# Kernel tuning notes

Hardware: AMD Instinct MI355X
Metric: run time of the kernel (lower is better)

## Reference

```python
import jax, jax.numpy as jnp
import numpy as np

B, D, P = 1024, 1024, 16  # batch, latent_dim(=out_dim), part_dim

def setup_inputs() -> dict:
    key = jax.random.key(0)
    k1, k2 = jax.random.split(key)
    x = jax.random.normal(k1, (B, D, P), dtype=jnp.float32)
    # per-part Linear weights, torch Linear weight shape [out, in] stacked over parts
    W = jax.random.normal(k2, (P, D, D), dtype=jnp.float32) * 0.02
    return {"x": x, "W": W}

def reference(x, W):
    # x: [B, D, P]; W: [P, O, D] (O == D here). stack_dim=-1: slice last dim,
    # apply part-specific Linear (no bias) + exact GELU, stack on last dim.
    y = jnp.einsum('bdp,pod->bop', x, W)  # grouped per-part GEMM -> [B, O, P]
    return jax.nn.gelu(y, approximate=False)
```

## Files before the change

kernel.cpp:

```cpp
#include <hip/hip_runtime.h>
#include <hip/hip_bf16.h>
#include <math.h>

typedef __hip_bfloat16 bf16;
typedef __attribute__((ext_vector_type(8))) short bf16x8;
typedef __attribute__((ext_vector_type(4))) float f32x4;
typedef __attribute__((ext_vector_type(16))) float f32x16;

#define DI static __device__ __forceinline__

constexpr int NB = 1024;
constexpr int ND = 1024;
constexpr int NP = 16;
constexpr int BKT = 32;
constexpr int NKT = ND / BKT;

DI float gelu_exact(float x) {
    return 0.5f * x * (1.0f + erff(x * 0.70710678118654752f));
}

DI ushort bf16_bits(float f) {
    bf16 h = __float2bfloat16(f);
    return *reinterpret_cast<ushort*>(&h);
}

__global__ __launch_bounds__(256) void pack_kernel(const float* __restrict__ x,
                                                   const float* __restrict__ w,
                                                   bf16* __restrict__ xp,
                                                   bf16* __restrict__ wp) {
    __shared__ ushort lds[16][264];
    const int t = threadIdx.x;
    if (blockIdx.x < 4096) {
        const int b = blockIdx.x >> 2;
        const int q = blockIdx.x & 3;
        const float* xb = x + ((size_t)b * ND + q * 256) * NP;
        float4 va[2], vb[2];
#pragma unroll
        for (int it = 0; it < 2; ++it) {
            const int u  = it * 256 + t;
            const int dh = u >> 2;
            const int p0 = (u & 3) * 4;
            va[it] = *reinterpret_cast<const float4*>(&xb[(size_t)(dh * 2)     * NP + p0]);
            vb[it] = *reinterpret_cast<const float4*>(&xb[(size_t)(dh * 2 + 1) * NP + p0]);
        }
#pragma unroll
        for (int it = 0; it < 2; ++it) {
            const int u  = it * 256 + t;
            const int dh = u >> 2;
            const int p0 = (u & 3) * 4;
            const float a0[4] = { va[it].x, va[it].y, va[it].z, va[it].w };
            const float a1[4] = { vb[it].x, vb[it].y, vb[it].z, vb[it].w };
#pragma unroll
            for (int k = 0; k < 4; ++k) {
                const uint packed = (uint)bf16_bits(a0[k]) | ((uint)bf16_bits(a1[k]) << 16);
                *reinterpret_cast<uint*>(&lds[p0 + k][dh * 2]) = packed;
            }
        }
        __syncthreads();
        const int p = t >> 4, j = t & 15;
        bf16* dst = xp + (size_t)p * (NB * ND) + (size_t)b * ND + q * 256;
#pragma unroll
        for (int it = 0; it < 2; ++it) {
            const int c = it * 16 + j;
            *reinterpret_cast<bf16x8*>(&dst[c * 8]) =
                *reinterpret_cast<const bf16x8*>(&lds[p][c * 8]);
        }
    } else {
        const size_t i = ((size_t)(blockIdx.x - 4096) * 256 + t) * 16;
        float4 f[4];
#pragma unroll
        for (int k = 0; k < 4; ++k)
            f[k] = *reinterpret_cast<const float4*>(&w[i + k * 4]);
#pragma unroll
        for (int h = 0; h < 2; ++h) {
            alignas(16) bf16 tmp[8] = {
                __float2bfloat16(f[h * 2].x),     __float2bfloat16(f[h * 2].y),
                __float2bfloat16(f[h * 2].z),     __float2bfloat16(f[h * 2].w),
                __float2bfloat16(f[h * 2 + 1].x), __float2bfloat16(f[h * 2 + 1].y),
                __float2bfloat16(f[h * 2 + 1].z), __float2bfloat16(f[h * 2 + 1].w) };
            *reinterpret_cast<bf16x8*>(&wp[i + h * 8]) = *reinterpret_cast<const bf16x8*>(tmp);
        }
    }
}

__global__ __launch_bounds__(512, 2) void gemm8_kernel(const bf16* __restrict__ xp,
                                                       const bf16* __restrict__ wp,
                                                       bf16* __restrict__ y) {
    __shared__ bf16 As[3][256 * BKT];
    __shared__ bf16 Bs[3][256 * BKT];
    const int i = blockIdx.x;
    const int p    = ((i & 7) << 1) | ((i >> 3) & 1);
    const int tile = i >> 4;
    const int bt = (tile >> 2) * 256;
    const int ot = (tile & 3) * 256;
    const bf16* A  = xp + (size_t)p * NB * ND;
    const bf16* Bm = wp + (size_t)p * ND * ND;
    const int t = threadIdx.x;
    const int l = t & 63, w = t >> 6;
    const int wr = w >> 2, wc = w & 3;
    const int lr32 = l & 31, g2 = l >> 5;

    f32x16 acc[4][2] = {};

    auto stage = [&](int buf, int kt, int q) {
        const int s   = ((q & 1) * 8 + w) * 64 + l;
        const int row = s >> 2;
        const int cb  = (s & 3) ^ ((row >> 1) & 3);
        const bf16* gsrc = (q < 2 ? A + (size_t)(bt + row) * ND
                                  : Bm + (size_t)(ot + row) * ND) + kt * BKT + cb * 8;
        bf16* ldst = (q < 2 ? &As[buf][((q & 1) * 8 + w) * 512]
                            : &Bs[buf][((q & 1) * 8 + w) * 512]);
        __builtin_amdgcn_global_load_lds((const __attribute__((address_space(1))) void*)gsrc,
                                         (__attribute__((address_space(3))) void*)ldst, 16, 0, 0);
    };
    auto readA = [&](int buf, int m, int s) -> bf16x8 {
        const int row  = wr * 128 + m * 32 + lr32;
        const int ch   = s * 2 + g2;
        const int slot = row * 4 + (ch ^ ((row >> 1) & 3));
        return *reinterpret_cast<const bf16x8*>(&As[buf][slot * 8]);
    };
    auto readB = [&](int buf, int n, int s) -> bf16x8 {
        const int row  = wc * 64 + n * 32 + lr32;
        const int ch   = s * 2 + g2;
        const int slot = row * 4 + (ch ^ ((row >> 1) & 3));
        return *reinterpret_cast<const bf16x8*>(&Bs[buf][slot * 8]);
    };

#pragma unroll
    for (int q = 0; q < 4; ++q) stage(0, 0, q);
#pragma unroll
    for (int q = 0; q < 4; ++q) stage(1, 1, q);
    asm volatile("s_waitcnt vmcnt(4)" ::: "memory");
    __builtin_amdgcn_s_barrier();
    __builtin_amdgcn_sched_barrier(0);

    int bufc = 0, bufs = 2;
#pragma unroll 1
    for (int kt = 0; kt < NKT; ++kt) {
        bf16x8 bfr[2], af[4];
#pragma unroll
        for (int n = 0; n < 2; ++n) bfr[n] = readB(bufc, n, 0);
#pragma unroll
        for (int m = 0; m < 4; ++m) af[m] = readA(bufc, m, 0);
        if (kt + 2 < NKT) { stage(bufs, kt + 2, 0); stage(bufs, kt + 2, 1); }
        __builtin_amdgcn_s_barrier();
        asm volatile("s_waitcnt lgkmcnt(0)" ::: "memory");
        __builtin_amdgcn_s_setprio(1);
#pragma unroll
        for (int m = 0; m < 4; ++m)
#pragma unroll
            for (int n = 0; n < 2; ++n)
                acc[m][n] = __builtin_amdgcn_mfma_f32_32x32x16_bf16(af[m], bfr[n], acc[m][n], 0, 0, 0);
        __builtin_amdgcn_s_setprio(0);
        __builtin_amdgcn_s_barrier();
#pragma unroll
        for (int n = 0; n < 2; ++n) bfr[n] = readB(bufc, n, 1);
#pragma unroll
        for (int m = 0; m < 4; ++m) af[m] = readA(bufc, m, 1);
        if (kt + 2 < NKT) { stage(bufs, kt + 2, 2); stage(bufs, kt + 2, 3); }
        __builtin_amdgcn_s_barrier();
        asm volatile("s_waitcnt lgkmcnt(0)" ::: "memory");
        __builtin_amdgcn_s_setprio(1);
#pragma unroll
        for (int m = 0; m < 4; ++m)
#pragma unroll
            for (int n = 0; n < 2; ++n)
                acc[m][n] = __builtin_amdgcn_mfma_f32_32x32x16_bf16(af[m], bfr[n], acc[m][n], 0, 0, 0);
        __builtin_amdgcn_s_setprio(0);
        if (kt < NKT - 1) {
            if (kt + 2 < NKT) asm volatile("s_waitcnt vmcnt(4)" ::: "memory");
            else              asm volatile("s_waitcnt vmcnt(0)" ::: "memory");
            __builtin_amdgcn_s_barrier();
            __builtin_amdgcn_sched_barrier(0);
        }
        bufc = (bufc == 2) ? 0 : bufc + 1;
        bufs = (bufs == 2) ? 0 : bufs + 1;
    }

    bf16* yp = y + (size_t)p * NB * ND;
#pragma unroll
    for (int m = 0; m < 4; ++m) {
#pragma unroll
        for (int n = 0; n < 2; ++n) {
#pragma unroll
            for (int reg = 0; reg < 16; ++reg) {
                const int row = bt + wr * 128 + m * 32 + (reg & 3) + 8 * (reg >> 2) + 4 * g2;
                const int col = ot + wc * 64 + n * 32 + lr32;
                yp[(size_t)row * ND + col] = __float2bfloat16(acc[m][n][reg]);
            }
        }
    }
}

__global__ __launch_bounds__(256) void unpack_kernel(const bf16* __restrict__ y,
                                                     float* __restrict__ out) {
    const size_t gidx = (size_t)blockIdx.x * 256 + threadIdx.x;
    const size_t o = gidx & 1023;
    const size_t b = gidx >> 10;
    const bf16* yb = y + b * (size_t)ND + o;
    float v[16];
#pragma unroll
    for (int p = 0; p < 16; ++p)
        v[p] = gelu_exact(__bfloat162float(yb[(size_t)p * (NB * ND)]));
    float4* dst = reinterpret_cast<float4*>(out + gidx * NP);
#pragma unroll
    for (int q = 0; q < 4; ++q)
        dst[q] = make_float4(v[q * 4], v[q * 4 + 1], v[q * 4 + 2], v[q * 4 + 3]);
}

__global__ __launch_bounds__(256, 4) void gemm_direct_kernel(const bf16* __restrict__ xp,
                                                             const bf16* __restrict__ wp,
                                                             float* __restrict__ out) {
    constexpr int BK = 32;
    __shared__ bf16 As[2][128 * BK];
    __shared__ bf16 Bs[2][128 * BK];
    const int i = blockIdx.x;
    const int p    = ((i & 7) << 1) | ((i >> 9) & 1);
    const int tile = (i >> 3) & 63;
    const int ot = (tile & 7) * 128;
    const int bt = (tile >> 3) * 128;
    const bf16* A  = xp + (size_t)p * NB * ND;
    const bf16* Bm = wp + (size_t)p * ND * ND;
    const int t = threadIdx.x;
    const int l = t & 63;
    const int w = t >> 6;
    const int wr = w >> 1, wc = w & 1;
    f32x4 acc[4][4] = {};
    auto stage = [&](int buf, int k0) {
#pragma unroll
        for (int r = 0; r < 2; ++r) {
            const int c   = r * 256 + t;
            const int row = c >> 2;
            const int cc  = c & 3;
            const bf16* ga = A  + (size_t)(bt + row) * ND + (k0 + cc * 8);
            const bf16* gb = Bm + (size_t)(ot + row) * ND + (k0 + cc * 8);
            bf16* la = &As[buf][(r * 256 + w * 64) * 8];
            bf16* lb = &Bs[buf][(r * 256 + w * 64) * 8];
            __builtin_amdgcn_global_load_lds((const __attribute__((address_space(1))) void*)ga,
                                             (__attribute__((address_space(3))) void*)la, 16, 0, 0);
            __builtin_amdgcn_global_load_lds((const __attribute__((address_space(1))) void*)gb,
                                             (__attribute__((address_space(3))) void*)lb, 16, 0, 0);
        }
    };
    int buf = 0;
    stage(0, 0);
    for (int kt = 0; kt < ND / BK; ++kt) {
        __syncthreads();
        if (kt + 1 < ND / BK) stage(buf ^ 1, (kt + 1) * BK);
        const int lr = l & 15;
        const int lk = (l >> 4) * 8;
        bf16x8 af[4], bfr[4];
#pragma unroll
        for (int m = 0; m < 4; ++m)
            af[m] = *reinterpret_cast<const bf16x8*>(&As[buf][(wr * 64 + m * 16 + lr) * BK + lk]);
#pragma unroll
        for (int n = 0; n < 4; ++n)
            bfr[n] = *reinterpret_cast<const bf16x8*>(&Bs[buf][(wc * 64 + n * 16 + lr) * BK + lk]);
#pragma unroll
        for (int m = 0; m < 4; ++m)
#pragma unroll
            for (int n = 0; n < 4; ++n)
                acc[m][n] = __builtin_amdgcn_mfma_f32_16x16x32_bf16(af[m], bfr[n], acc[m][n], 0, 0, 0);
        buf ^= 1;
    }
    const int lr4 = (l >> 4) * 4;
    const int lc  = l & 15;
    const int row0 = bt + wr * 64, col0 = ot + wc * 64;
#pragma unroll
    for (int m = 0; m < 4; ++m)
#pragma unroll
        for (int j = 0; j < 4; ++j) {
            const int r = row0 + m * 16 + lr4 + j;
#pragma unroll
            for (int n = 0; n < 4; ++n) {
                const int c = col0 + n * 16 + lc;
                out[((size_t)r * ND + c) * NP + p] = gelu_exact(acc[m][n][j]);
            }
        }
}

__global__ __launch_bounds__(256) void fallback_kernel(const float* __restrict__ x,
                                                       const float* __restrict__ w,
                                                       float* __restrict__ out) {
    __shared__ float As[64][17];
    __shared__ float Bs[64][17];
    const int p = blockIdx.z, bt = blockIdx.y * 64, ot = blockIdx.x * 64;
    const int t = threadIdx.x;
    const int tx = t & 15, ty = t >> 4;
    float acc[4][4] = {};
    for (int k0 = 0; k0 < ND; k0 += 16) {
        __syncthreads();
#pragma unroll
        for (int i = 0; i < 4; ++i) {
            const int idx = i * 256 + t;
            const int r = idx >> 4, k = idx & 15;
            As[r][k] = x[((size_t)(bt + r) * ND + k0 + k) * NP + p];
            Bs[r][k] = w[(size_t)p * ND * ND + (size_t)(ot + r) * ND + k0 + k];
        }
        __syncthreads();
#pragma unroll
        for (int k = 0; k < 16; ++k) {
            float a[4], bb[4];
#pragma unroll
            for (int i = 0; i < 4; ++i) a[i] = As[ty * 4 + i][k];
#pragma unroll
            for (int j = 0; j < 4; ++j) bb[j] = Bs[tx * 4 + j][k];
#pragma unroll
            for (int i = 0; i < 4; ++i)
#pragma unroll
                for (int j = 0; j < 4; ++j) acc[i][j] += a[i] * bb[j];
        }
    }
#pragma unroll
    for (int i = 0; i < 4; ++i)
#pragma unroll
        for (int j = 0; j < 4; ++j)
            out[((size_t)(bt + ty * 4 + i) * ND + (ot + tx * 4 + j)) * NP + p] =
                gelu_exact(acc[i][j]);
}

extern "C" void kernel_launch(void* const* d_in, const int* in_sizes, int n_in,
                              void* d_out, int out_size, void* d_ws, size_t ws_size,
                              hipStream_t stream) {
    const float* x = (const float*)d_in[0];
    const float* w = (const float*)d_in[1];
    float* out = (float*)d_out;

    const size_t nElem     = (size_t)NP * NB * ND;
    const size_t packBytes = nElem * sizeof(bf16) * 2;
    const size_t yBytes    = nElem * sizeof(bf16);

    if (ws_size >= packBytes) {
        bf16* xp = (bf16*)d_ws;
        bf16* wp = xp + nElem;
        pack_kernel<<<8192, 256, 0, stream>>>(x, w, xp, wp);
        if (ws_size >= packBytes + yBytes) {
            bf16* y = (bf16*)((char*)d_ws + packBytes);
            gemm8_kernel<<<256, 512, 0, stream>>>(xp, wp, y);
            unpack_kernel<<<(int)(NB * ND / 256), 256, 0, stream>>>(y, out);
        } else {
            gemm_direct_kernel<<<1024, 256, 0, stream>>>(xp, wp, out);
        }
    } else {
        fallback_kernel<<<dim3(16, 16, 16), 256, 0, stream>>>(x, w, out);
    }
}
```

Measured before the change: 112.7 us.

## Fuse weight fp32-to-bf16 conversion into GEMM B-tile staging

Drops the separate weight-packing pass. The GEMM now loads fp32 weights straight into registers, converts them to bf16, and writes them into the swizzled LDS tile, one stage ahead through two ping-pong register sets. This removes a full write and re-read of a 32MB bf16 copy of W. In exchange each GEMM block reads twice as many bytes for B, and the extra register pressure forces launch_bounds occupancy from 2 to 1.

```diff
diff --git a/kernel.cpp b/kernel.cpp
--- a/kernel.cpp
+++ b/kernel.cpp
@@ -25,66 +25,47 @@
 }
 
 __global__ __launch_bounds__(256) void pack_kernel(const float* __restrict__ x,
-                                                   const float* __restrict__ w,
-                                                   bf16* __restrict__ xp,
-                                                   bf16* __restrict__ wp) {
+                                                   bf16* __restrict__ xp) {
     __shared__ ushort lds[16][264];
     const int t = threadIdx.x;
-    if (blockIdx.x < 4096) {
-        const int b = blockIdx.x >> 2;
-        const int q = blockIdx.x & 3;
-        const float* xb = x + ((size_t)b * ND + q * 256) * NP;
-        float4 va[2], vb[2];
-#pragma unroll
-        for (int it = 0; it < 2; ++it) {
-            const int u  = it * 256 + t;
-            const int dh = u >> 2;
-            const int p0 = (u & 3) * 4;
-            va[it] = *reinterpret_cast<const float4*>(&xb[(size_t)(dh * 2)     * NP + p0]);
-            vb[it] = *reinterpret_cast<const float4*>(&xb[(size_t)(dh * 2 + 1) * NP + p0]);
-        }
-#pragma unroll
-        for (int it = 0; it < 2; ++it) {
-            const int u  = it * 256 + t;
-            const int dh = u >> 2;
-            const int p0 = (u & 3) * 4;
-            const float a0[4] = { va[it].x, va[it].y, va[it].z, va[it].w };
-            const float a1[4] = { vb[it].x, vb[it].y, vb[it].z, vb[it].w };
-#pragma unroll
-            for (int k = 0; k < 4; ++k) {
-                const uint packed = (uint)bf16_bits(a0[k]) | ((uint)bf16_bits(a1[k]) << 16);
-                *reinterpret_cast<uint*>(&lds[p0 + k][dh * 2]) = packed;
-            }
-        }
-        __syncthreads();
-        const int p = t >> 4, j = t & 15;
-        bf16* dst = xp + (size_t)p * (NB * ND) + (size_t)b * ND + q * 256;
-#pragma unroll
-        for (int it = 0; it < 2; ++it) {
-            const int c = it * 16 + j;
-            *reinterpret_cast<bf16x8*>(&dst[c * 8]) =
-                *reinterpret_cast<const bf16x8*>(&lds[p][c * 8]);
-        }
-    } else {
-        const size_t i = ((size_t)(blockIdx.x - 4096) * 256 + t) * 16;
-        float4 f[4];
-#pragma unroll
-        for (int k = 0; k < 4; ++k)
-            f[k] = *reinterpret_cast<const float4*>(&w[i + k * 4]);
-#pragma unroll
-        for (int h = 0; h < 2; ++h) {
-            alignas(16) bf16 tmp[8] = {
-                __float2bfloat16(f[h * 2].x),     __float2bfloat16(f[h * 2].y),
-                __float2bfloat16(f[h * 2].z),     __float2bfloat16(f[h * 2].w),
-                __float2bfloat16(f[h * 2 + 1].x), __float2bfloat16(f[h * 2 + 1].y),
-                __float2bfloat16(f[h * 2 + 1].z), __float2bfloat16(f[h * 2 + 1].w) };
-            *reinterpret_cast<bf16x8*>(&wp[i + h * 8]) = *reinterpret_cast<const bf16x8*>(tmp);
-        }
-    }
-}
-
-__global__ __launch_bounds__(512, 2) void gemm8_kernel(const bf16* __restrict__ xp,
-                                                       const bf16* __restrict__ wp,
+    const int b = blockIdx.x >> 2;
+    const int q = blockIdx.x & 3;
+    const float* xb = x + ((size_t)b * ND + q * 256) * NP;
+    float4 va[2], vb[2];
+#pragma unroll
+    for (int it = 0; it < 2; ++it) {
+        const int u  = it * 256 + t;
+        const int dh = u >> 2;
+        const int p0 = (u & 3) * 4;
+        va[it] = *reinterpret_cast<const float4*>(&xb[(size_t)(dh * 2)     * NP + p0]);
+        vb[it] = *reinterpret_cast<const float4*>(&xb[(size_t)(dh * 2 + 1) * NP + p0]);
+    }
+#pragma unroll
+    for (int it = 0; it < 2; ++it) {
+        const int u  = it * 256 + t;
+        const int dh = u >> 2;
+        const int p0 = (u & 3) * 4;
+        const float a0[4] = { va[it].x, va[it].y, va[it].z, va[it].w };
+        const float a1[4] = { vb[it].x, vb[it].y, vb[it].z, vb[it].w };
+#pragma unroll
+        for (int k = 0; k < 4; ++k) {
+            const uint packed = (uint)bf16_bits(a0[k]) | ((uint)bf16_bits(a1[k]) << 16);
+            *reinterpret_cast<uint*>(&lds[p0 + k][dh * 2]) = packed;
+        }
+    }
+    __syncthreads();
+    const int p = t >> 4, j = t & 15;
+    bf16* dst = xp + (size_t)p * (NB * ND) + (size_t)b * ND + q * 256;
+#pragma unroll
+    for (int it = 0; it < 2; ++it) {
+        const int c = it * 16 + j;
+        *reinterpret_cast<bf16x8*>(&dst[c * 8]) =
+            *reinterpret_cast<const bf16x8*>(&lds[p][c * 8]);
+    }
+}
+
+__global__ __launch_bounds__(512, 1) void gemm8_kernel(const bf16* __restrict__ xp,
+                                                       const float* __restrict__ wsrc,
                                                        bf16* __restrict__ y) {
     __shared__ bf16 As[3][256 * BKT];
     __shared__ bf16 Bs[3][256 * BKT];
@@ -93,25 +74,47 @@
     const int tile = i >> 4;
     const int bt = (tile >> 2) * 256;
     const int ot = (tile & 3) * 256;
-    const bf16* A  = xp + (size_t)p * NB * ND;
-    const bf16* Bm = wp + (size_t)p * ND * ND;
+    const bf16*  A  = xp   + (size_t)p * NB * ND;
+    const float* Bm = wsrc + (size_t)p * ND * ND;
     const int t = threadIdx.x;
     const int l = t & 63, w = t >> 6;
     const int wr = w >> 2, wc = w & 3;
     const int lr32 = l & 31, g2 = l >> 5;
 
     f32x16 acc[4][2] = {};
-
-    auto stage = [&](int buf, int kt, int q) {
-        const int s   = ((q & 1) * 8 + w) * 64 + l;
+    float4 bregA[4], bregB[4];
+
+    const int sA = w * 64 + l;
+
+    auto issueA = [&](int buf, int kt, int q) {
+        const int s   = (q * 8 + w) * 64 + l;
         const int row = s >> 2;
         const int cb  = (s & 3) ^ ((row >> 1) & 3);
-        const bf16* gsrc = (q < 2 ? A + (size_t)(bt + row) * ND
-                                  : Bm + (size_t)(ot + row) * ND) + kt * BKT + cb * 8;
-        bf16* ldst = (q < 2 ? &As[buf][((q & 1) * 8 + w) * 512]
-                            : &Bs[buf][((q & 1) * 8 + w) * 512]);
+        const bf16* gsrc = A + (size_t)(bt + row) * ND + kt * BKT + cb * 8;
+        bf16* ldst = &As[buf][(q * 8 + w) * 512];
         __builtin_amdgcn_global_load_lds((const __attribute__((address_space(1))) void*)gsrc,
                                          (__attribute__((address_space(3))) void*)ldst, 16, 0, 0);
+    };
+    auto issueB = [&](int kt, float4 (&r)[4]) {
+#pragma unroll
+        for (int i2 = 0; i2 < 4; ++i2) {
+            const int g   = i2 * 512 + sA;
+            const int row = g >> 3, o16 = g & 7;
+            r[i2] = *reinterpret_cast<const float4*>(&Bm[(size_t)(ot + row) * ND + kt * BKT + o16 * 4]);
+        }
+    };
+    auto writeB = [&](int buf, const float4 (&r)[4]) {
+#pragma unroll
+        for (int i2 = 0; i2 < 4; ++i2) {
+            const int g   = i2 * 512 + sA;
+            const int row = g >> 3, o16 = g & 7;
+            const int ch = o16 >> 1, h8 = o16 & 1;
+            alignas(8) bf16 tmp[4] = { __float2bfloat16(r[i2].x), __float2bfloat16(r[i2].y),
+                                       __float2bfloat16(r[i2].z), __float2bfloat16(r[i2].w) };
+            const int slot = row * 4 + (ch ^ ((row >> 1) & 3));
+            *reinterpret_cast<uint2*>(&Bs[buf][slot * 8 + h8 * 4]) =
+                *reinterpret_cast<const uint2*>(tmp);
+        }
     };
     auto readA = [&](int buf, int m, int s) -> bf16x8 {
         const int row  = wr * 128 + m * 32 + lr32;
@@ -126,23 +129,28 @@
         return *reinterpret_cast<const bf16x8*>(&Bs[buf][slot * 8]);
     };
 
-#pragma unroll
-    for (int q = 0; q < 4; ++q) stage(0, 0, q);
-#pragma unroll
-    for (int q = 0; q < 4; ++q) stage(1, 1, q);
-    asm volatile("s_waitcnt vmcnt(4)" ::: "memory");
+    issueB(0, bregA); issueA(0, 0, 0); issueA(0, 0, 1);
+    issueB(1, bregB); issueA(1, 1, 0); issueA(1, 1, 1);
+    asm volatile("s_waitcnt vmcnt(6)" ::: "memory");
+    writeB(0, bregA);
+    asm volatile("s_waitcnt lgkmcnt(0)" ::: "memory");
     __builtin_amdgcn_s_barrier();
     __builtin_amdgcn_sched_barrier(0);
 
-    int bufc = 0, bufs = 2;
 #pragma unroll 1
     for (int kt = 0; kt < NKT; ++kt) {
+        const int c  = kt % 3;
+        const int n1 = (kt + 1) % 3;
+        const int s2 = (kt + 2) % 3;
         bf16x8 bfr[2], af[4];
 #pragma unroll
-        for (int n = 0; n < 2; ++n) bfr[n] = readB(bufc, n, 0);
-#pragma unroll
-        for (int m = 0; m < 4; ++m) af[m] = readA(bufc, m, 0);
-        if (kt + 2 < NKT) { stage(bufs, kt + 2, 0); stage(bufs, kt + 2, 1); }
+        for (int n = 0; n < 2; ++n) bfr[n] = readB(c, n, 0);
+#pragma unroll
+        for (int m = 0; m < 4; ++m) af[m] = readA(c, m, 0);
+        if (kt + 2 < NKT) {
+            if ((kt & 1) == 0) issueB(kt + 2, bregA);
+            else               issueB(kt + 2, bregB);
+        }
         __builtin_amdgcn_s_barrier();
         asm volatile("s_waitcnt lgkmcnt(0)" ::: "memory");
         __builtin_amdgcn_s_setprio(1);
@@ -154,10 +162,10 @@
         __builtin_amdgcn_s_setprio(0);
         __builtin_amdgcn_s_barrier();
 #pragma unroll
-        for (int n = 0; n < 2; ++n) bfr[n] = readB(bufc, n, 1);
-#pragma unroll
-        for (int m = 0; m < 4; ++m) af[m] = readA(bufc, m, 1);
-        if (kt + 2 < NKT) { stage(bufs, kt + 2, 2); stage(bufs, kt + 2, 3); }
+        for (int n = 0; n < 2; ++n) bfr[n] = readB(c, n, 1);
+#pragma unroll
+        for (int m = 0; m < 4; ++m) af[m] = readA(c, m, 1);
+        if (kt + 2 < NKT) { issueA(s2, kt + 2, 0); issueA(s2, kt + 2, 1); }
         __builtin_amdgcn_s_barrier();
         asm volatile("s_waitcnt lgkmcnt(0)" ::: "memory");
         __builtin_amdgcn_s_setprio(1);
@@ -167,14 +175,15 @@
             for (int n = 0; n < 2; ++n)
                 acc[m][n] = __builtin_amdgcn_mfma_f32_32x32x16_bf16(af[m], bfr[n], acc[m][n], 0, 0, 0);
         __builtin_amdgcn_s_setprio(0);
-        if (kt < NKT - 1) {
-            if (kt + 2 < NKT) asm volatile("s_waitcnt vmcnt(4)" ::: "memory");
+        if (kt + 1 < NKT) {
+            if (kt + 2 < NKT) asm volatile("s_waitcnt vmcnt(6)" ::: "memory");
             else              asm volatile("s_waitcnt vmcnt(0)" ::: "memory");
+            if (((kt + 1) & 1) == 0) writeB(n1, bregA);
+            else                     writeB(n1, bregB);
+            asm volatile("s_waitcnt lgkmcnt(0)" ::: "memory");
             __builtin_amdgcn_s_barrier();
             __builtin_amdgcn_sched_barrier(0);
         }
-        bufc = (bufc == 2) ? 0 : bufc + 1;
-        bufs = (bufs == 2) ? 0 : bufs + 1;
     }
 
     bf16* yp = y + (size_t)p * NB * ND;
@@ -206,77 +215,6 @@
 #pragma unroll
     for (int q = 0; q < 4; ++q)
         dst[q] = make_float4(v[q * 4], v[q * 4 + 1], v[q * 4 + 2], v[q * 4 + 3]);
-}
-
-__global__ __launch_bounds__(256, 4) void gemm_direct_kernel(const bf16* __restrict__ xp,
-                                                             const bf16* __restrict__ wp,
-                                                             float* __restrict__ out) {
-    constexpr int BK = 32;
-    __shared__ bf16 As[2][128 * BK];
-    __shared__ bf16 Bs[2][128 * BK];
-    const int i = blockIdx.x;
-    const int p    = ((i & 7) << 1) | ((i >> 9) & 1);
-    const int tile = (i >> 3) & 63;
-    const int ot = (tile & 7) * 128;
-    const int bt = (tile >> 3) * 128;
-    const bf16* A  = xp + (size_t)p * NB * ND;
-    const bf16* Bm = wp + (size_t)p * ND * ND;
-    const int t = threadIdx.x;
-    const int l = t & 63;
-    const int w = t >> 6;
-    const int wr = w >> 1, wc = w & 1;
-    f32x4 acc[4][4] = {};
-    auto stage = [&](int buf, int k0) {
-#pragma unroll
-        for (int r = 0; r < 2; ++r) {
-            const int c   = r * 256 + t;
-            const int row = c >> 2;
-            const int cc  = c & 3;
-            const bf16* ga = A  + (size_t)(bt + row) * ND + (k0 + cc * 8);
-            const bf16* gb = Bm + (size_t)(ot + row) * ND + (k0 + cc * 8);
-            bf16* la = &As[buf][(r * 256 + w * 64) * 8];
-            bf16* lb = &Bs[buf][(r * 256 + w * 64) * 8];
-            __builtin_amdgcn_global_load_lds((const __attribute__((address_space(1))) void*)ga,
-                                             (__attribute__((address_space(3))) void*)la, 16, 0, 0);
-            __builtin_amdgcn_global_load_lds((const __attribute__((address_space(1))) void*)gb,
-                                             (__attribute__((address_space(3))) void*)lb, 16, 0, 0);
-        }
-    };
-    int buf = 0;
-    stage(0, 0);
-    for (int kt = 0; kt < ND / BK; ++kt) {
-        __syncthreads();
-        if (kt + 1 < ND / BK) stage(buf ^ 1, (kt + 1) * BK);
-        const int lr = l & 15;
-        const int lk = (l >> 4) * 8;
-        bf16x8 af[4], bfr[4];
-#pragma unroll
-        for (int m = 0; m < 4; ++m)
-            af[m] = *reinterpret_cast<const bf16x8*>(&As[buf][(wr * 64 + m * 16 + lr) * BK + lk]);
-#pragma unroll
-        for (int n = 0; n < 4; ++n)
-            bfr[n] = *reinterpret_cast<const bf16x8*>(&Bs[buf][(wc * 64 + n * 16 + lr) * BK + lk]);
-#pragma unroll
-        for (int m = 0; m < 4; ++m)
-#pragma unroll
-            for (int n = 0; n < 4; ++n)
-                acc[m][n] = __builtin_amdgcn_mfma_f32_16x16x32_bf16(af[m], bfr[n], acc[m][n], 0, 0, 0);
-        buf ^= 1;
-    }
-    const int lr4 = (l >> 4) * 4;
-    const int lc  = l & 15;
-    const int row0 = bt + wr * 64, col0 = ot + wc * 64;
-#pragma unroll
-    for (int m = 0; m < 4; ++m)
-#pragma unroll
-        for (int j = 0; j < 4; ++j) {
-            const int r = row0 + m * 16 + lr4 + j;
-#pragma unroll
-            for (int n = 0; n < 4; ++n) {
-                const int c = col0 + n * 16 + lc;
-                out[((size_t)r * ND + c) * NP + p] = gelu_exact(acc[m][n][j]);
-            }
-        }
 }
 
 __global__ __launch_bounds__(256) void fallback_kernel(const float* __restrict__ x,
@@ -326,21 +264,16 @@
     const float* w = (const float*)d_in[1];
     float* out = (float*)d_out;
 
-    const size_t nElem     = (size_t)NP * NB * ND;
-    const size_t packBytes = nElem * sizeof(bf16) * 2;
-    const size_t yBytes    = nElem * sizeof(bf16);
-
-    if (ws_size >= packBytes) {
+    const size_t nElem  = (size_t)NP * NB * ND;
+    const size_t xpB    = nElem * sizeof(bf16);
+    const size_t yB     = nElem * sizeof(bf16);
+
+    if (ws_size >= xpB + yB) {
         bf16* xp = (bf16*)d_ws;
-        bf16* wp = xp + nElem;
-        pack_kernel<<<8192, 256, 0, stream>>>(x, w, xp, wp);
-        if (ws_size >= packBytes + yBytes) {
-            bf16* y = (bf16*)((char*)d_ws + packBytes);
-            gemm8_kernel<<<256, 512, 0, stream>>>(xp, wp, y);
-            unpack_kernel<<<(int)(NB * ND / 256), 256, 0, stream>>>(y, out);
-        } else {
-            gemm_direct_kernel<<<1024, 256, 0, stream>>>(xp, wp, out);
-        }
+        bf16* y  = (bf16*)((char*)d_ws + xpB);
+        pack_kernel<<<4096, 256, 0, stream>>>(x, xp);
+        gemm8_kernel<<<256, 512, 0, stream>>>(xp, w, y);
+        unpack_kernel<<<(int)(NB * ND / 256), 256, 0, stream>>>(y, out);
     } else {
         fallback_kernel<<<dim3(16, 16, 16), 256, 0, stream>>>(x, w, out);
     }
```

Result: slower. 117.6 us (+4.4%).
